# Kernel tuning notes

Hardware: AMD Instinct MI355X
Metric: run time of the kernel (lower is better)

## Reference

```python
import jax, jax.numpy as jnp
import numpy as np

NUM_LAYERS = 2  # layer 0 = lstm_in; layers 1..L-1 all share lstm_middle weights


def _cell(x, h, c, w_ih, w_hh, b_ih, b_hh):
    gates = x @ w_ih.T + h @ w_hh.T + b_ih + b_hh  # [B, 4H]
    i, f, g, o = jnp.split(gates, 4, axis=-1)
    i = jax.nn.sigmoid(i)
    f = jax.nn.sigmoid(f)
    g = jnp.tanh(g)
    o = jax.nn.sigmoid(o)
    c = f * c + i * g
    h = o * jnp.tanh(c)
    return h, c, jnp.stack([i, f, g, o])  # gates of this layer: [4, B, H]


def _run_direction(xs, p_in, p_mid):
    # xs: [T, B, I] (already reversed for the backward pass)
    T, B, _ = xs.shape
    H = p_in[1].shape[1]
    init = (jnp.zeros((NUM_LAYERS, B, H), xs.dtype), jnp.zeros((NUM_LAYERS, B, H), xs.dtype))

    def step(carry, x):
        hs, cs = carry
        inp = x
        nh, nc = [], []
        g = None
        for l in range(NUM_LAYERS):
            p = p_in if l == 0 else p_mid
            h, c, g = _cell(inp, hs[l], cs[l], *p)
            # dropout(p=0.1) on non-final layers is identity in eval mode
            nh.append(h)
            nc.append(c)
            inp = h
        return (jnp.stack(nh), jnp.stack(nc)), (inp, g, nc[-1])

    _, (outs, gates, cells) = jax.lax.scan(step, init, xs)
    return outs, gates, cells  # [T,B,H], [T,4,B,H], [T,B,H]


def setup_inputs() -> dict:
    key = jax.random.key(0)
    ks = jax.random.split(key, 12)
    B, T, I, H, O = 32, 512, 256, 512, 256
    s_i, s_h = 1.0 / np.sqrt(I), 1.0 / np.sqrt(H)
    return {
        "inputs": jax.random.normal(ks[0], (B, T, I), jnp.float32),
        "w_ih_in": jax.random.normal(ks[1], (4 * H, I), jnp.float32) * s_i,
        "w_hh_in": jax.random.normal(ks[2], (4 * H, H), jnp.float32) * s_h,
        "b_ih_in": jax.random.normal(ks[3], (4 * H,), jnp.float32) * s_h,
        "b_hh_in": jax.random.normal(ks[4], (4 * H,), jnp.float32) * s_h,
        "w_ih_mid": jax.random.normal(ks[5], (4 * H, H), jnp.float32) * s_h,
        "w_hh_mid": jax.random.normal(ks[6], (4 * H, H), jnp.float32) * s_h,
        "b_ih_mid": jax.random.normal(ks[7], (4 * H,), jnp.float32) * s_h,
        "b_hh_mid": jax.random.normal(ks[8], (4 * H,), jnp.float32) * s_h,
        "fc_w": jax.random.normal(ks[9], (O, 2 * H), jnp.float32) * (1.0 / np.sqrt(2 * H)),
        "fc_b": jax.random.normal(ks[10], (O,), jnp.float32) * 0.01,
    }


def reference(inputs, w_ih_in, w_hh_in, b_ih_in, b_hh_in,
              w_ih_mid, w_hh_mid, b_ih_mid, b_hh_mid, fc_w, fc_b):
    p_in = (w_ih_in, w_hh_in, b_ih_in, b_hh_in)
    p_mid = (w_ih_mid, w_hh_mid, b_ih_mid, b_hh_mid)
    xs = jnp.transpose(inputs, (1, 0, 2))  # [T, B, I]
    of, gf, cf = _run_direction(xs, p_in, p_mid)
    # backward pass: scanning over reversed xs yields results already indexed
    # by forward_seq_idx = T-1-seq_idx, matching the original concat ordering
    ob, gb, cb = _run_direction(xs[::-1], p_in, p_mid)
    out = jnp.concatenate([of, ob], axis=-1)       # [T, B, 2H]
    gates = jnp.concatenate([gf, gb], axis=-1)     # [T, 4, B, 2H]
    hn = jnp.concatenate([cf, cb], axis=-1)        # [T, B, 2H]
    y = out @ fc_w.T + fc_b                        # [T, B, O]
    y = jnp.transpose(y, (1, 0, 2))                # [B, T, O]
    return y, gates, hn
```

## Files before the change

kernel.cpp:

```cpp
#include <hip/hip_runtime.h>
#include <hip/hip_bf16.h>
#include <stdint.h>

#define TT 512
#define BB 32
#define II 256
#define HH 512
#define OO 256
#define N4H 2048
#define CL_WGS 64
#define UPW 8
#define NCOL 32

typedef __attribute__((ext_vector_type(8))) short bf16x8;
typedef __attribute__((ext_vector_type(4))) float f32x4;

static __device__ __forceinline__ f32x4 MFMA(bf16x8 a, bf16x8 b, f32x4 c) {
  return __builtin_amdgcn_mfma_f32_16x16x32_bf16(a, b, c, 0, 0, 0);
}
static __device__ __forceinline__ unsigned short f2bf(float x) {
  union { float f; unsigned u; } v; v.f = x;
  unsigned r = v.u + 0x7FFFu + ((v.u >> 16) & 1u);
  return (unsigned short)(r >> 16);
}
static __device__ __forceinline__ float bf2f(unsigned short b) {
  union { unsigned u; float f; } v; v.u = ((unsigned)b) << 16; return v.f;
}
static __device__ __forceinline__ float sigm(float x) {
  return 1.0f / (1.0f + __expf(-x));
}
static __device__ __forceinline__ float tanh_(float x) {
  return 1.0f - 2.0f / (1.0f + __expf(2.0f * x));
}


__global__ void prep_w(const float* __restrict__ src, unsigned short* __restrict__ hi,
                       unsigned short* __restrict__ lo, int K, int N, int packed) {
  int tid = blockIdx.x * 256 + threadIdx.x;
  int nch = K >> 3;
  if (tid >= N * nch) return;
  int c = tid / nch;
  int j = (tid - c * nch) << 3;
  int row = packed ? ((c & 3) * HH + (c >> 2)) : c;
  const float* s = src + (size_t)row * K + j;
  alignas(16) unsigned short h8[8];
  alignas(16) unsigned short l8[8];
#pragma unroll
  for (int e = 0; e < 8; ++e) {
    float v = s[e];
    unsigned short hb = f2bf(v);
    h8[e] = hb;
    l8[e] = f2bf(v - bf2f(hb));
  }
  *(uint4*)(hi + (size_t)c * K + j) = *(const uint4*)h8;
  *(uint4*)(lo + (size_t)c * K + j) = *(const uint4*)l8;
}

__global__ void prep_bias(const float* __restrict__ bi0, const float* __restrict__ bh0,
                          const float* __restrict__ bim, const float* __restrict__ bhm,
                          float* __restrict__ bias0p, float* __restrict__ biasmp) {
  int c = blockIdx.x * 256 + threadIdx.x;
  if (c >= N4H) return;
  int row = (c & 3) * HH + (c >> 2);
  bias0p[c] = bi0[row] + bh0[row];
  biasmp[c] = bim[row] + bhm[row];
}

__global__ void prep_x(const float* __restrict__ in, unsigned short* __restrict__ xb) {
  int tid = blockIdx.x * 256 + threadIdx.x;
  if (tid >= 16384 * 32) return;
  int row = tid >> 5, j = (tid & 31) << 3;
  int t = row >> 5, b = row & 31;
  const float* s = in + ((size_t)b * TT + t) * II + j;
  alignas(16) unsigned short o8[8];
#pragma unroll
  for (int e = 0; e < 8; ++e) o8[e] = f2bf(s[e]);
  *(uint4*)(xb + (size_t)row * II + j) = *(const uint4*)o8;
}


__global__ __launch_bounds__(256) void gemm_g0(
    const unsigned short* __restrict__ A, const unsigned short* __restrict__ Bhi,
    const unsigned short* __restrict__ Blo, const float* __restrict__ biasp,
    float* __restrict__ out) {
  const int K = II;
  int wgm = blockIdx.x & 255;
  int wgn = blockIdx.x >> 8;
  int l = threadIdx.x & 63, wave = threadIdx.x >> 6;
  int mbase = wgm * 64 + wave * 16;
  int nbase = wgn * 64;
  int arow = mbase + (l & 15);
  int koff = (l >> 4) * 8;
  f32x4 acc[4] = {};
  for (int kt = 0; kt < K / 32; ++kt) {
    bf16x8 a = *(const bf16x8*)(A + (size_t)arow * K + kt * 32 + koff);
#pragma unroll
    for (int n = 0; n < 4; ++n) {
      int col = nbase + n * 16 + (l & 15);
      bf16x8 bh = *(const bf16x8*)(Bhi + (size_t)col * K + kt * 32 + koff);
      bf16x8 bl = *(const bf16x8*)(Blo + (size_t)col * K + kt * 32 + koff);
      acc[n] = MFMA(a, bh, acc[n]);
      acc[n] = MFMA(a, bl, acc[n]);
    }
  }
#pragma unroll
  for (int n = 0; n < 4; ++n) {
    int col = nbase + n * 16 + (l & 15);
    float bv = biasp[col];
#pragma unroll
    for (int r = 0; r < 4; ++r) {
      int row = mbase + (l >> 4) * 4 + r;
      out[(size_t)row * N4H + col] = acc[n][r] + bv;
    }
  }
}

__global__ __launch_bounds__(256) void gemm_fc(
    const unsigned short* __restrict__ A, const unsigned short* __restrict__ Bhi,
    const unsigned short* __restrict__ Blo, const float* __restrict__ bias,
    float* __restrict__ y) {
  const int K = 2 * HH;
  int wgm = blockIdx.x & 255;
  int wgn = blockIdx.x >> 8;
  int l = threadIdx.x & 63, wave = threadIdx.x >> 6;
  int mbase = wgm * 64 + wave * 16;
  int nbase = wgn * 64;
  int arow = mbase + (l & 15);
  int koff = (l >> 4) * 8;
  f32x4 acc[4] = {};
  for (int kt = 0; kt < K / 32; ++kt) {
    bf16x8 a = *(const bf16x8*)(A + (size_t)arow * K + kt * 32 + koff);
#pragma unroll
    for (int n = 0; n < 4; ++n) {
      int col = nbase + n * 16 + (l & 15);
      bf16x8 bh = *(const bf16x8*)(Bhi + (size_t)col * K + kt * 32 + koff);
      bf16x8 bl = *(const bf16x8*)(Blo + (size_t)col * K + kt * 32 + koff);
      acc[n] = MFMA(a, bh, acc[n]);
      acc[n] = MFMA(a, bl, acc[n]);
    }
  }
#pragma unroll
  for (int n = 0; n < 4; ++n) {
    int col = nbase + n * 16 + (l & 15);
    float bv = bias[col];
#pragma unroll
    for (int r = 0; r < 4; ++r) {
      int row = mbase + (l >> 4) * 4 + r;
      int t = row >> 5, b = row & 31;
      y[((size_t)b * TT + t) * OO + col] = acc[n][r] + bv;
    }
  }
}


static __device__ void stage_w_lds(const unsigned short* __restrict__ g, int c0,
                                   unsigned short* __restrict__ lds) {
  int cl = threadIdx.x >> 3;
  int sub = threadIdx.x & 7;
  const uint4* src = (const uint4*)(g + (size_t)(c0 + cl) * HH);
  for (int j = sub; j < 64; j += 8) {
    uint4 v = src[j];
    int off = cl * 1024 + ((j ^ (cl & 7)) << 4);
    *(uint4*)((char*)lds + off) = v;
  }
}
static __device__ __forceinline__ bf16x8 lds_bfrag(const unsigned short* lds, int cl, int kc) {
  int off = cl * 1024 + ((kc ^ (cl & 7)) << 4);
  return *(const bf16x8*)((const char*)lds + off);
}
static __device__ __forceinline__ void cluster_wait(unsigned int* f, unsigned tgt) {
  if (threadIdx.x < CL_WGS) {
    while (true) {
      unsigned v = __hip_atomic_load(f + threadIdx.x, __ATOMIC_RELAXED, __HIP_MEMORY_SCOPE_AGENT);
      if (__all((int)(v >= tgt))) break;
    }
  }
  __syncthreads();
}

__global__ void __launch_bounds__(256, 1) scan_l0(
    const unsigned short* __restrict__ Whi, const unsigned short* __restrict__ Wlo,
    const float* __restrict__ g0x, unsigned short* __restrict__ h0,
    unsigned int* __restrict__ flags) {
  extern __shared__ char smem[];
  unsigned short* whi = (unsigned short*)smem;
  unsigned short* wlo = (unsigned short*)(smem + 32768);
  unsigned short* hst = (unsigned short*)(smem + 65536);
  const int dir = blockIdx.x >> 6;
  const int wg = blockIdx.x & 63;
  const int tid = threadIdx.x;
  const int l = tid & 63;
  const int wave = tid >> 6;
  stage_w_lds(Whi, wg * NCOL, whi);
  stage_w_lds(Wlo, wg * NCOL, wlo);
  __syncthreads();
  const int mt = wave & 1, nt = wave >> 1;
  const int lc = nt * 16 + (l & 15);
  const int gate = lc & 3;
  const int ulocal = lc >> 2;
  const int rowb = mt * 16 + ((l >> 4) << 2);
  const int arow = mt * 16 + (l & 15);
  const int koff = (l >> 4) * 8;
  unsigned int* myf = flags + dir * CL_WGS;
  float cprev[4] = {0.f, 0.f, 0.f, 0.f};
  for (int t = 0; t < TT; ++t) {
    const int tin = dir ? (TT - 1 - t) : t;
    float gx[4];
#pragma unroll
    for (int r = 0; r < 4; ++r)
      gx[r] = g0x[((size_t)tin * BB + rowb + r) * N4H + wg * NCOL + lc];
    f32x4 acc0 = {}, acc1 = {};
    if (t > 0) {
      cluster_wait(myf, (unsigned)t);
      const unsigned short* hp =
          h0 + (size_t)(dir * TT + (t - 1)) * BB * HH + (size_t)arow * HH + koff;
#pragma unroll
      for (int kt = 0; kt < 16; ++kt) {
        bf16x8 a = *(const bf16x8*)(hp + kt * 32);
        acc0 = MFMA(a, lds_bfrag(whi, lc, kt * 4 + (l >> 4)), acc0);
        acc1 = MFMA(a, lds_bfrag(wlo, lc, kt * 4 + (l >> 4)), acc1);
      }
    }
    float hnew[4];
#pragma unroll
    for (int r = 0; r < 4; ++r) {
      float pre = acc0[r] + acc1[r] + gx[r];
      float own = (gate == 2) ? tanh_(pre) : sigm(pre);
      int q = l & 60;
      float iv = __shfl(own, q + 0, 64);
      float fv = __shfl(own, q + 1, 64);
      float gv = __shfl(own, q + 2, 64);
      float ov = __shfl(own, q + 3, 64);
      float cn = fv * cprev[r] + iv * gv;
      cprev[r] = cn;
      hnew[r] = ov * tanh_(cn);
    }
    if (gate == 0) {
#pragma unroll
      for (int r = 0; r < 4; ++r) hst[(rowb + r) * UPW + ulocal] = f2bf(hnew[r]);
    }
    __syncthreads();
    if (tid < 64) {
      unsigned long long v = *(const unsigned long long*)(hst + tid * 4);
      size_t off = ((size_t)(dir * TT + t) * BB + (tid >> 1)) * HH + wg * UPW + (tid & 1) * 4;
      __hip_atomic_store((unsigned long long*)(h0 + off), v, __ATOMIC_RELAXED,
                         __HIP_MEMORY_SCOPE_AGENT);
    }
    __syncthreads();
    if (tid == 0)
      __hip_atomic_store(myf + wg, (unsigned)(t + 1), __ATOMIC_RELAXED, __HIP_MEMORY_SCOPE_AGENT);
  }
}

__global__ void __launch_bounds__(256, 1) scan_l1(
    const unsigned short* __restrict__ Xhi, const unsigned short* __restrict__ Xlo,
    const unsigned short* __restrict__ Rhi, const unsigned short* __restrict__ Rlo,
    const unsigned short* __restrict__ h0, const float* __restrict__ biasp,
    unsigned short* __restrict__ out1, float* __restrict__ gates, float* __restrict__ hn,
    unsigned int* __restrict__ flags) {
  extern __shared__ char smem[];
  unsigned short* xhi = (unsigned short*)smem;
  unsigned short* xlo = (unsigned short*)(smem + 32768);
  unsigned short* rhi = (unsigned short*)(smem + 65536);
  unsigned short* rlo = (unsigned short*)(smem + 98304);
  unsigned short* hst = (unsigned short*)(smem + 131072);
  const int dir = blockIdx.x >> 6;
  const int wg = blockIdx.x & 63;
  const int tid = threadIdx.x;
  const int l = tid & 63;
  const int wave = tid >> 6;
  stage_w_lds(Xhi, wg * NCOL, xhi);
  stage_w_lds(Xlo, wg * NCOL, xlo);
  stage_w_lds(Rhi, wg * NCOL, rhi);
  stage_w_lds(Rlo, wg * NCOL, rlo);
  __syncthreads();
  const int mt = wave & 1, nt = wave >> 1;
  const int lc = nt * 16 + (l & 15);
  const int gate = lc & 3;
  const int ulocal = lc >> 2;
  const int ug = wg * UPW + ulocal;
  const int rowb = mt * 16 + ((l >> 4) << 2);
  const int arow = mt * 16 + (l & 15);
  const int koff = (l >> 4) * 8;
  unsigned int* myf = flags + dir * CL_WGS;
  const float bias = biasp[wg * NCOL + lc];
  float cprev[4] = {0.f, 0.f, 0.f, 0.f};
  for (int t = 0; t < TT; ++t) {
    f32x4 acc0 = {}, acc1 = {};
    {
      const unsigned short* xp =
          h0 + (size_t)(dir * TT + t) * BB * HH + (size_t)arow * HH + koff;
#pragma unroll
      for (int kt = 0; kt < 16; ++kt) {
        bf16x8 a = *(const bf16x8*)(xp + kt * 32);
        acc0 = MFMA(a, lds_bfrag(xhi, lc, kt * 4 + (l >> 4)), acc0);
        acc1 = MFMA(a, lds_bfrag(xlo, lc, kt * 4 + (l >> 4)), acc1);
      }
    }
    if (t > 0) {
      cluster_wait(myf, (unsigned)t);
      const unsigned short* hp = out1 + (size_t)(t - 1) * BB * 2 * HH +
                                 (size_t)arow * 2 * HH + dir * HH + koff;
#pragma unroll
      for (int kt = 0; kt < 16; ++kt) {
        bf16x8 a = *(const bf16x8*)(hp + kt * 32);
        acc0 = MFMA(a, lds_bfrag(rhi, lc, kt * 4 + (l >> 4)), acc0);
        acc1 = MFMA(a, lds_bfrag(rlo, lc, kt * 4 + (l >> 4)), acc1);
      }
    }
    float hnew[4];
#pragma unroll
    for (int r = 0; r < 4; ++r) {
      float pre = acc0[r] + acc1[r] + bias;
      float own = (gate == 2) ? tanh_(pre) : sigm(pre);
      gates[(((size_t)t * 4 + gate) * BB + rowb + r) * (2 * HH) + dir * HH + ug] = own;
      int q = l & 60;
      float iv = __shfl(own, q + 0, 64);
      float fv = __shfl(own, q + 1, 64);
      float gv = __shfl(own, q + 2, 64);
      float ov = __shfl(own, q + 3, 64);
      float cn = fv * cprev[r] + iv * gv;
      cprev[r] = cn;
      if (gate == 1) hn[((size_t)t * BB + rowb + r) * (2 * HH) + dir * HH + ug] = cn;
      hnew[r] = ov * tanh_(cn);
    }
    if (gate == 0) {
#pragma unroll
      for (int r = 0; r < 4; ++r) hst[(rowb + r) * UPW + ulocal] = f2bf(hnew[r]);
    }
    __syncthreads();
    if (tid < 64) {
      unsigned long long v = *(const unsigned long long*)(hst + tid * 4);
      size_t off = ((size_t)t * BB + (tid >> 1)) * (2 * HH) + dir * HH + wg * UPW + (tid & 1) * 4;
      __hip_atomic_store((unsigned long long*)(out1 + off), v, __ATOMIC_RELAXED,
                         __HIP_MEMORY_SCOPE_AGENT);
    }
    __syncthreads();
    if (tid == 0)
      __hip_atomic_store(myf + wg, (unsigned)(t + 1), __ATOMIC_RELAXED, __HIP_MEMORY_SCOPE_AGENT);
  }
}

extern "C" void kernel_launch(void* const* d_in, const int* in_sizes, int n_in,
                              void* d_out, int out_size, void* d_ws, size_t ws_size,
                              hipStream_t stream) {
  const float* inputs   = (const float*)d_in[0];
  const float* w_ih_in  = (const float*)d_in[1];
  const float* w_hh_in  = (const float*)d_in[2];
  const float* b_ih_in  = (const float*)d_in[3];
  const float* b_hh_in  = (const float*)d_in[4];
  const float* w_ih_mid = (const float*)d_in[5];
  const float* w_hh_mid = (const float*)d_in[6];
  const float* b_ih_mid = (const float*)d_in[7];
  const float* b_hh_mid = (const float*)d_in[8];
  const float* fc_w     = (const float*)d_in[9];
  const float* fc_b     = (const float*)d_in[10];

  char* p = (char*)d_ws;
  auto take = [&](size_t n) { char* q = p; p += (n + 255) & ~(size_t)255; return q; };
  unsigned short* xb        = (unsigned short*)take((size_t)16384 * II * 2);
  unsigned short* wihin_hi  = (unsigned short*)take((size_t)N4H * II * 2);
  unsigned short* wihin_lo  = (unsigned short*)take((size_t)N4H * II * 2);
  unsigned short* whhin_hi  = (unsigned short*)take((size_t)N4H * HH * 2);
  unsigned short* whhin_lo  = (unsigned short*)take((size_t)N4H * HH * 2);
  unsigned short* wihmid_hi = (unsigned short*)take((size_t)N4H * HH * 2);
  unsigned short* wihmid_lo = (unsigned short*)take((size_t)N4H * HH * 2);
  unsigned short* whhmid_hi = (unsigned short*)take((size_t)N4H * HH * 2);
  unsigned short* whhmid_lo = (unsigned short*)take((size_t)N4H * HH * 2);
  unsigned short* fchi      = (unsigned short*)take((size_t)OO * 2 * HH * 2);
  unsigned short* fclo      = (unsigned short*)take((size_t)OO * 2 * HH * 2);
  float* bias0p             = (float*)take((size_t)N4H * 4);
  float* biasmp             = (float*)take((size_t)N4H * 4);
  float* g0x                = (float*)take((size_t)16384 * N4H * 4);
  unsigned short* h0        = (unsigned short*)take((size_t)2 * TT * BB * HH * 2);
  unsigned short* out1      = (unsigned short*)take((size_t)TT * BB * 2 * HH * 2);
  unsigned int* flags       = (unsigned int*)take(4096);

  float* y_out     = (float*)d_out;
  float* gates_out = y_out + (size_t)BB * TT * OO;
  float* hn_out    = gates_out + (size_t)TT * 4 * BB * 2 * HH;

  hipMemsetAsync(flags, 0, 4096, stream);
  hipFuncSetAttribute(reinterpret_cast<const void*>(scan_l0),
                      hipFuncAttributeMaxDynamicSharedMemorySize, 90112);
  hipFuncSetAttribute(reinterpret_cast<const void*>(scan_l1),
                      hipFuncAttributeMaxDynamicSharedMemorySize, 131584);

  prep_w<<<256, 256, 0, stream>>>(w_ih_in, wihin_hi, wihin_lo, II, N4H, 1);
  prep_w<<<512, 256, 0, stream>>>(w_hh_in, whhin_hi, whhin_lo, HH, N4H, 1);
  prep_w<<<512, 256, 0, stream>>>(w_ih_mid, wihmid_hi, wihmid_lo, HH, N4H, 1);
  prep_w<<<512, 256, 0, stream>>>(w_hh_mid, whhmid_hi, whhmid_lo, HH, N4H, 1);
  prep_w<<<128, 256, 0, stream>>>(fc_w, fchi, fclo, 2 * HH, OO, 0);
  prep_bias<<<8, 256, 0, stream>>>(b_ih_in, b_hh_in, b_ih_mid, b_hh_mid, bias0p, biasmp);
  prep_x<<<2048, 256, 0, stream>>>(inputs, xb);
  gemm_g0<<<8192, 256, 0, stream>>>(xb, wihin_hi, wihin_lo, bias0p, g0x);
  scan_l0<<<128, 256, 90112, stream>>>(whhin_hi, whhin_lo, g0x, h0, flags);
  scan_l1<<<128, 256, 131584, stream>>>(wihmid_hi, wihmid_lo, whhmid_hi, whhmid_lo, h0, biasmp,
                                        out1, gates_out, hn_out, flags + 128);
  gemm_fc<<<1024, 256, 0, stream>>>(out1, fchi, fclo, fc_b, y_out);
}
```

Measured before the change: 6.479 ms.

## Fuse layer-0 and layer-1 scans into one wavefront-pipelined persistent kernel

Replaces the two sequential scan kernels with one 256-block kernel. Blocks 0-127 run the layer-0 recurrence while blocks 128-255 run layer 1, each layer-1 step waiting on per-step flags from layer 0, so the two layers overlap in a wavefront instead of running back to back. Weights move from LDS into registers (64 bf16x8 per lane for layer 1). Each lane now writes its hidden value with a single atomic store instead of staging through LDS. The risks are high register pressure or spills, all 256 blocks having to be co-resident to avoid deadlock, and extra polling traffic.

```diff
diff --git a/kernel.cpp b/kernel.cpp
--- a/kernel.cpp
+++ b/kernel.cpp
@@ -8,9 +8,6 @@
 #define HH 512
 #define OO 256
 #define N4H 2048
-#define CL_WGS 64
-#define UPW 8
-#define NCOL 32
 
 typedef __attribute__((ext_vector_type(8))) short bf16x8;
 typedef __attribute__((ext_vector_type(4))) float f32x4;
@@ -153,191 +150,166 @@
 }
 
 
-static __device__ void stage_w_lds(const unsigned short* __restrict__ g, int c0,
-                                   unsigned short* __restrict__ lds) {
-  int cl = threadIdx.x >> 3;
-  int sub = threadIdx.x & 7;
-  const uint4* src = (const uint4*)(g + (size_t)(c0 + cl) * HH);
-  for (int j = sub; j < 64; j += 8) {
-    uint4 v = src[j];
-    int off = cl * 1024 + ((j ^ (cl & 7)) << 4);
-    *(uint4*)((char*)lds + off) = v;
-  }
-}
-static __device__ __forceinline__ bf16x8 lds_bfrag(const unsigned short* lds, int cl, int kc) {
-  int off = cl * 1024 + ((kc ^ (cl & 7)) << 4);
-  return *(const bf16x8*)((const char*)lds + off);
-}
-static __device__ __forceinline__ void cluster_wait(unsigned int* f, unsigned tgt) {
-  if (threadIdx.x < CL_WGS) {
-    while (true) {
-      unsigned v = __hip_atomic_load(f + threadIdx.x, __ATOMIC_RELAXED, __HIP_MEMORY_SCOPE_AGENT);
-      if (__all((int)(v >= tgt))) break;
-    }
-  }
-  __syncthreads();
-}
-
-__global__ void __launch_bounds__(256, 1) scan_l0(
-    const unsigned short* __restrict__ Whi, const unsigned short* __restrict__ Wlo,
-    const float* __restrict__ g0x, unsigned short* __restrict__ h0,
+static __device__ __forceinline__ void wait1(const unsigned* f, unsigned tgt) {
+  const int l = threadIdx.x & 63;
+  while (true) {
+    unsigned v = __hip_atomic_load(f + l, __ATOMIC_RELAXED, __HIP_MEMORY_SCOPE_AGENT);
+    if (__all((int)(v >= tgt))) break;
+  }
+  __threadfence();
+}
+static __device__ __forceinline__ void wait2(const unsigned* a, unsigned ta,
+                                             const unsigned* b, unsigned tb) {
+  const int l = threadIdx.x & 63;
+  while (true) {
+    unsigned va = __hip_atomic_load(a + l, __ATOMIC_RELAXED, __HIP_MEMORY_SCOPE_AGENT);
+    unsigned vb = __hip_atomic_load(b + l, __ATOMIC_RELAXED, __HIP_MEMORY_SCOPE_AGENT);
+    if (__all((int)((va >= ta) && (vb >= tb)))) break;
+  }
+  __threadfence();
+}
+
+__global__ void __launch_bounds__(256, 1) scan_fused(
+    const unsigned short* __restrict__ W0hi, const unsigned short* __restrict__ W0lo,
+    const unsigned short* __restrict__ Xhi, const unsigned short* __restrict__ Xlo,
+    const unsigned short* __restrict__ Rhi, const unsigned short* __restrict__ Rlo,
+    const float* __restrict__ g0x, const float* __restrict__ biasmp,
+    unsigned short* __restrict__ h0, unsigned short* __restrict__ out1,
+    float* __restrict__ gates, float* __restrict__ hn,
     unsigned int* __restrict__ flags) {
-  extern __shared__ char smem[];
-  unsigned short* whi = (unsigned short*)smem;
-  unsigned short* wlo = (unsigned short*)(smem + 32768);
-  unsigned short* hst = (unsigned short*)(smem + 65536);
-  const int dir = blockIdx.x >> 6;
-  const int wg = blockIdx.x & 63;
+  const int bid = blockIdx.x;
+  const int cid = bid >> 6;
+  const int wg = bid & 63;
+  const int dir = cid & 1;
   const int tid = threadIdx.x;
   const int l = tid & 63;
   const int wave = tid >> 6;
-  stage_w_lds(Whi, wg * NCOL, whi);
-  stage_w_lds(Wlo, wg * NCOL, wlo);
-  __syncthreads();
-  const int mt = wave & 1, nt = wave >> 1;
-  const int lc = nt * 16 + (l & 15);
-  const int gate = lc & 3;
-  const int ulocal = lc >> 2;
-  const int rowb = mt * 16 + ((l >> 4) << 2);
-  const int arow = mt * 16 + (l & 15);
-  const int koff = (l >> 4) * 8;
-  unsigned int* myf = flags + dir * CL_WGS;
-  float cprev[4] = {0.f, 0.f, 0.f, 0.f};
-  for (int t = 0; t < TT; ++t) {
-    const int tin = dir ? (TT - 1 - t) : t;
-    float gx[4];
-#pragma unroll
-    for (int r = 0; r < 4; ++r)
-      gx[r] = g0x[((size_t)tin * BB + rowb + r) * N4H + wg * NCOL + lc];
-    f32x4 acc0 = {}, acc1 = {};
-    if (t > 0) {
-      cluster_wait(myf, (unsigned)t);
-      const unsigned short* hp =
-          h0 + (size_t)(dir * TT + (t - 1)) * BB * HH + (size_t)arow * HH + koff;
+  const int cg = wave & 1;
+  const int rg = wave >> 1;
+  const int col = wg * 32 + cg * 16 + (l & 15);
+  const int gate = col & 3;
+  const int ug = col >> 2;
+  const int kq = (l >> 4) * 8;
+  const int q = l & 60;
+  const int arow = rg * 16 + (l & 15);
+  const int crow = rg * 16 + (l >> 4) * 4;
+  const int srow = crow + (l & 3);
+  unsigned int* myf = flags + cid * 64;
+  unsigned short* hbase = h0 + (size_t)dir * TT * BB * HH;
+
+  if (cid < 2) {
+    bf16x8 wr_h[16], wr_l[16];
+    {
+      const unsigned short* p1 = W0hi + (size_t)col * HH + kq;
+      const unsigned short* p2 = W0lo + (size_t)col * HH + kq;
 #pragma unroll
       for (int kt = 0; kt < 16; ++kt) {
-        bf16x8 a = *(const bf16x8*)(hp + kt * 32);
-        acc0 = MFMA(a, lds_bfrag(whi, lc, kt * 4 + (l >> 4)), acc0);
-        acc1 = MFMA(a, lds_bfrag(wlo, lc, kt * 4 + (l >> 4)), acc1);
-      }
-    }
-    float hnew[4];
-#pragma unroll
-    for (int r = 0; r < 4; ++r) {
-      float pre = acc0[r] + acc1[r] + gx[r];
-      float own = (gate == 2) ? tanh_(pre) : sigm(pre);
-      int q = l & 60;
-      float iv = __shfl(own, q + 0, 64);
-      float fv = __shfl(own, q + 1, 64);
-      float gv = __shfl(own, q + 2, 64);
-      float ov = __shfl(own, q + 3, 64);
-      float cn = fv * cprev[r] + iv * gv;
-      cprev[r] = cn;
-      hnew[r] = ov * tanh_(cn);
-    }
-    if (gate == 0) {
-#pragma unroll
-      for (int r = 0; r < 4; ++r) hst[(rowb + r) * UPW + ulocal] = f2bf(hnew[r]);
-    }
-    __syncthreads();
-    if (tid < 64) {
-      unsigned long long v = *(const unsigned long long*)(hst + tid * 4);
-      size_t off = ((size_t)(dir * TT + t) * BB + (tid >> 1)) * HH + wg * UPW + (tid & 1) * 4;
-      __hip_atomic_store((unsigned long long*)(h0 + off), v, __ATOMIC_RELAXED,
-                         __HIP_MEMORY_SCOPE_AGENT);
-    }
-    __syncthreads();
-    if (tid == 0)
-      __hip_atomic_store(myf + wg, (unsigned)(t + 1), __ATOMIC_RELAXED, __HIP_MEMORY_SCOPE_AGENT);
-  }
-}
-
-__global__ void __launch_bounds__(256, 1) scan_l1(
-    const unsigned short* __restrict__ Xhi, const unsigned short* __restrict__ Xlo,
-    const unsigned short* __restrict__ Rhi, const unsigned short* __restrict__ Rlo,
-    const unsigned short* __restrict__ h0, const float* __restrict__ biasp,
-    unsigned short* __restrict__ out1, float* __restrict__ gates, float* __restrict__ hn,
-    unsigned int* __restrict__ flags) {
-  extern __shared__ char smem[];
-  unsigned short* xhi = (unsigned short*)smem;
-  unsigned short* xlo = (unsigned short*)(smem + 32768);
-  unsigned short* rhi = (unsigned short*)(smem + 65536);
-  unsigned short* rlo = (unsigned short*)(smem + 98304);
-  unsigned short* hst = (unsigned short*)(smem + 131072);
-  const int dir = blockIdx.x >> 6;
-  const int wg = blockIdx.x & 63;
-  const int tid = threadIdx.x;
-  const int l = tid & 63;
-  const int wave = tid >> 6;
-  stage_w_lds(Xhi, wg * NCOL, xhi);
-  stage_w_lds(Xlo, wg * NCOL, xlo);
-  stage_w_lds(Rhi, wg * NCOL, rhi);
-  stage_w_lds(Rlo, wg * NCOL, rlo);
-  __syncthreads();
-  const int mt = wave & 1, nt = wave >> 1;
-  const int lc = nt * 16 + (l & 15);
-  const int gate = lc & 3;
-  const int ulocal = lc >> 2;
-  const int ug = wg * UPW + ulocal;
-  const int rowb = mt * 16 + ((l >> 4) << 2);
-  const int arow = mt * 16 + (l & 15);
-  const int koff = (l >> 4) * 8;
-  unsigned int* myf = flags + dir * CL_WGS;
-  const float bias = biasp[wg * NCOL + lc];
-  float cprev[4] = {0.f, 0.f, 0.f, 0.f};
-  for (int t = 0; t < TT; ++t) {
-    f32x4 acc0 = {}, acc1 = {};
+        wr_h[kt] = *(const bf16x8*)(p1 + kt * 32);
+        wr_l[kt] = *(const bf16x8*)(p2 + kt * 32);
+      }
+    }
+    float cprev[4] = {0.f, 0.f, 0.f, 0.f};
+    for (int t = 0; t < TT; ++t) {
+      const int tin = dir ? (TT - 1 - t) : t;
+      f32x4 acc;
+      const float* gp = g0x + ((size_t)tin * BB + crow) * N4H + col;
+#pragma unroll
+      for (int r = 0; r < 4; ++r) acc[r] = gp[(size_t)r * N4H];
+      if (t > 0) {
+        wait1(myf, (unsigned)t);
+        const unsigned short* ap = hbase + ((size_t)(t - 1) * BB + arow) * HH + kq;
+#pragma unroll
+        for (int kt = 0; kt < 16; ++kt) {
+          bf16x8 a = *(const bf16x8*)(ap + kt * 32);
+          acc = MFMA(a, wr_h[kt], acc);
+          acc = MFMA(a, wr_l[kt], acc);
+        }
+      }
+      float hsel = 0.f;
+#pragma unroll
+      for (int r = 0; r < 4; ++r) {
+        float pre = acc[r];
+        float own = (gate == 2) ? tanh_(pre) : sigm(pre);
+        float iv = __shfl(own, q + 0, 64);
+        float fv = __shfl(own, q + 1, 64);
+        float gv = __shfl(own, q + 2, 64);
+        float ov = __shfl(own, q + 3, 64);
+        float cn = fv * cprev[r] + iv * gv;
+        cprev[r] = cn;
+        float hv = ov * tanh_(cn);
+        if ((l & 3) == r) hsel = hv;
+      }
+      __hip_atomic_store(hbase + ((size_t)t * BB + srow) * HH + ug, f2bf(hsel),
+                         __ATOMIC_RELAXED, __HIP_MEMORY_SCOPE_AGENT);
+      __syncthreads();
+      if (tid == 0)
+        __hip_atomic_store(myf + wg, (unsigned)(t + 1), __ATOMIC_RELAXED,
+                           __HIP_MEMORY_SCOPE_AGENT);
+    }
+  } else {
+    const unsigned* l0f = flags + (cid - 2) * 64;
+    bf16x8 wx_h[16], wx_l[16], wr_h[16], wr_l[16];
     {
-      const unsigned short* xp =
-          h0 + (size_t)(dir * TT + t) * BB * HH + (size_t)arow * HH + koff;
+      const unsigned short* p1 = Xhi + (size_t)col * HH + kq;
+      const unsigned short* p2 = Xlo + (size_t)col * HH + kq;
+      const unsigned short* p3 = Rhi + (size_t)col * HH + kq;
+      const unsigned short* p4 = Rlo + (size_t)col * HH + kq;
 #pragma unroll
       for (int kt = 0; kt < 16; ++kt) {
-        bf16x8 a = *(const bf16x8*)(xp + kt * 32);
-        acc0 = MFMA(a, lds_bfrag(xhi, lc, kt * 4 + (l >> 4)), acc0);
-        acc1 = MFMA(a, lds_bfrag(xlo, lc, kt * 4 + (l >> 4)), acc1);
-      }
-    }
-    if (t > 0) {
-      cluster_wait(myf, (unsigned)t);
-      const unsigned short* hp = out1 + (size_t)(t - 1) * BB * 2 * HH +
-                                 (size_t)arow * 2 * HH + dir * HH + koff;
-#pragma unroll
-      for (int kt = 0; kt < 16; ++kt) {
-        bf16x8 a = *(const bf16x8*)(hp + kt * 32);
-        acc0 = MFMA(a, lds_bfrag(rhi, lc, kt * 4 + (l >> 4)), acc0);
-        acc1 = MFMA(a, lds_bfrag(rlo, lc, kt * 4 + (l >> 4)), acc1);
-      }
-    }
-    float hnew[4];
-#pragma unroll
-    for (int r = 0; r < 4; ++r) {
-      float pre = acc0[r] + acc1[r] + bias;
-      float own = (gate == 2) ? tanh_(pre) : sigm(pre);
-      gates[(((size_t)t * 4 + gate) * BB + rowb + r) * (2 * HH) + dir * HH + ug] = own;
-      int q = l & 60;
-      float iv = __shfl(own, q + 0, 64);
-      float fv = __shfl(own, q + 1, 64);
-      float gv = __shfl(own, q + 2, 64);
-      float ov = __shfl(own, q + 3, 64);
-      float cn = fv * cprev[r] + iv * gv;
-      cprev[r] = cn;
-      if (gate == 1) hn[((size_t)t * BB + rowb + r) * (2 * HH) + dir * HH + ug] = cn;
-      hnew[r] = ov * tanh_(cn);
-    }
-    if (gate == 0) {
-#pragma unroll
-      for (int r = 0; r < 4; ++r) hst[(rowb + r) * UPW + ulocal] = f2bf(hnew[r]);
-    }
-    __syncthreads();
-    if (tid < 64) {
-      unsigned long long v = *(const unsigned long long*)(hst + tid * 4);
-      size_t off = ((size_t)t * BB + (tid >> 1)) * (2 * HH) + dir * HH + wg * UPW + (tid & 1) * 4;
-      __hip_atomic_store((unsigned long long*)(out1 + off), v, __ATOMIC_RELAXED,
-                         __HIP_MEMORY_SCOPE_AGENT);
-    }
-    __syncthreads();
-    if (tid == 0)
-      __hip_atomic_store(myf + wg, (unsigned)(t + 1), __ATOMIC_RELAXED, __HIP_MEMORY_SCOPE_AGENT);
+        wx_h[kt] = *(const bf16x8*)(p1 + kt * 32);
+        wx_l[kt] = *(const bf16x8*)(p2 + kt * 32);
+        wr_h[kt] = *(const bf16x8*)(p3 + kt * 32);
+        wr_l[kt] = *(const bf16x8*)(p4 + kt * 32);
+      }
+    }
+    const float bias = biasmp[col];
+    float cprev[4] = {0.f, 0.f, 0.f, 0.f};
+    for (int t = 0; t < TT; ++t) {
+      wait2(l0f, (unsigned)(t + 1), myf, (unsigned)t);
+      f32x4 accx = {}, accr = {};
+      if (t > 0) {
+        const unsigned short* rp =
+            out1 + ((size_t)(t - 1) * BB + arow) * (2 * HH) + dir * HH + kq;
+#pragma unroll
+        for (int kt = 0; kt < 16; ++kt) {
+          bf16x8 a = *(const bf16x8*)(rp + kt * 32);
+          accr = MFMA(a, wr_h[kt], accr);
+          accr = MFMA(a, wr_l[kt], accr);
+        }
+      }
+      {
+        const unsigned short* ap = hbase + ((size_t)t * BB + arow) * HH + kq;
+#pragma unroll
+        for (int kt = 0; kt < 16; ++kt) {
+          bf16x8 a = *(const bf16x8*)(ap + kt * 32);
+          accx = MFMA(a, wx_h[kt], accx);
+          accx = MFMA(a, wx_l[kt], accx);
+        }
+      }
+      float hsel = 0.f;
+#pragma unroll
+      for (int r = 0; r < 4; ++r) {
+        float pre = accx[r] + accr[r] + bias;
+        float own = (gate == 2) ? tanh_(pre) : sigm(pre);
+        gates[(((size_t)t * 4 + gate) * BB + crow + r) * (2 * HH) + dir * HH + ug] = own;
+        float iv = __shfl(own, q + 0, 64);
+        float fv = __shfl(own, q + 1, 64);
+        float gv = __shfl(own, q + 2, 64);
+        float ov = __shfl(own, q + 3, 64);
+        float cn = fv * cprev[r] + iv * gv;
+        cprev[r] = cn;
+        if (gate == 1)
+          hn[((size_t)t * BB + crow + r) * (2 * HH) + dir * HH + ug] = cn;
+        float hv = ov * tanh_(cn);
+        if ((l & 3) == r) hsel = hv;
+      }
+      __hip_atomic_store(out1 + ((size_t)t * BB + srow) * (2 * HH) + dir * HH + ug,
+                         f2bf(hsel), __ATOMIC_RELAXED, __HIP_MEMORY_SCOPE_AGENT);
+      __syncthreads();
+      if (tid == 0)
+        __hip_atomic_store(myf + wg, (unsigned)(t + 1), __ATOMIC_RELAXED,
+                           __HIP_MEMORY_SCOPE_AGENT);
+    }
   }
 }
 
@@ -381,10 +353,6 @@
   float* hn_out    = gates_out + (size_t)TT * 4 * BB * 2 * HH;
 
   hipMemsetAsync(flags, 0, 4096, stream);
-  hipFuncSetAttribute(reinterpret_cast<const void*>(scan_l0),
-                      hipFuncAttributeMaxDynamicSharedMemorySize, 90112);
-  hipFuncSetAttribute(reinterpret_cast<const void*>(scan_l1),
-                      hipFuncAttributeMaxDynamicSharedMemorySize, 131584);
 
   prep_w<<<256, 256, 0, stream>>>(w_ih_in, wihin_hi, wihin_lo, II, N4H, 1);
   prep_w<<<512, 256, 0, stream>>>(w_hh_in, whhin_hi, whhin_lo, HH, N4H, 1);
@@ -394,8 +362,8 @@
   prep_bias<<<8, 256, 0, stream>>>(b_ih_in, b_hh_in, b_ih_mid, b_hh_mid, bias0p, biasmp);
   prep_x<<<2048, 256, 0, stream>>>(inputs, xb);
   gemm_g0<<<8192, 256, 0, stream>>>(xb, wihin_hi, wihin_lo, bias0p, g0x);
-  scan_l0<<<128, 256, 90112, stream>>>(whhin_hi, whhin_lo, g0x, h0, flags);
-  scan_l1<<<128, 256, 131584, stream>>>(wihmid_hi, wihmid_lo, whhmid_hi, whhmid_lo, h0, biasmp,
-                                        out1, gates_out, hn_out, flags + 128);
+  scan_fused<<<256, 256, 0, stream>>>(whhin_hi, whhin_lo, wihmid_hi, wihmid_lo,
+                                      whhmid_hi, whhmid_lo, g0x, biasmp, h0, out1,
+                                      gates_out, hn_out, flags);
   gemm_fc<<<1024, 256, 0, stream>>>(out1, fchi, fclo, fc_b, y_out);
 }
```

After: 14.21 ms. +119.3%, slower.
